# Kernel tuning notes

Hardware: AMD Instinct MI355X
Metric: run time of the kernel (lower is better)

Reference implementation:

```python
import jax, jax.numpy as jnp
import numpy as np

GAMMA = 0.1
N_CENTERS = 1024
INPUT_DIM = 64
BATCH = 65536


def setup_inputs() -> dict:
    key = jax.random.key(0)
    kx, kc = jax.random.split(key)
    x = jax.random.normal(kx, (BATCH, INPUT_DIM), dtype=jnp.float32)
    # centers ~ Uniform(0, 1), matching torch.empty(...).uniform_(0, 1)
    centers = jax.random.uniform(kc, (N_CENTERS, INPUT_DIM), dtype=jnp.float32)
    return {"x": x, "centers": centers}


def reference(x, centers):
    # Pairwise squared L2 distance via the matmul expansion trick:
    x_sq = jnp.sum(x * x, axis=-1, keepdims=True)          # [B, 1]
    c_sq = jnp.sum(centers * centers, axis=-1)             # [N]
    cross = jnp.einsum("bd,nd->bn", x, centers)            # [B, N]
    l2 = x_sq + c_sq[None, :] - 2.0 * cross                # [B, N]
    l2 = jnp.maximum(l2, 0.0)  # guard tiny negatives from the expansion
    return jnp.exp(-GAMMA * l2)
```

## Files before the change

### kernel.cpp

```cpp
#include <hip/hip_runtime.h>

#define GAMMA 0.1f

constexpr int MTOT = 65536;
constexpr int NTOT = 1024;
constexpr int KDIM = 64;
constexpr int RPB  = 256;
constexpr int SUB  = 64;
constexpr int NSUB = RPB / SUB;

using f16x8 = __attribute__((ext_vector_type(8))) _Float16;
using f16x4 = __attribute__((ext_vector_type(4))) _Float16;
using f32x4 = __attribute__((ext_vector_type(4))) float;

typedef __attribute__((address_space(1))) const unsigned int gu32;
typedef __attribute__((address_space(3))) unsigned int lu32;

constexpr size_t WS_CEN = 0;
constexpr size_t WS_CSQ = 131072;

__global__ __launch_bounds__(256)
void cen_convert_kernel(const float* __restrict__ centers,
                        _Float16* __restrict__ cen,
                        float* __restrict__ sq) {
  const int c = blockIdx.x * 256 + threadIdx.x;
  const int row = c >> 3;
  const int s = c & 7;
  const float4* p = reinterpret_cast<const float4*>(centers + (size_t)row * KDIM + s * 8);
  float4 v0 = p[0], v1 = p[1];
  const float v[8] = {v0.x, v0.y, v0.z, v0.w, v1.x, v1.y, v1.z, v1.w};
  f16x8 hv;
  float ss = 0.0f;
  #pragma unroll
  for (int i = 0; i < 8; ++i) {
    hv[i] = (_Float16)v[i];
    ss += v[i] * v[i];
  }
  ss += __shfl_xor(ss, 1);
  ss += __shfl_xor(ss, 2);
  ss += __shfl_xor(ss, 4);
  if (s == 0) sq[row] = ss;
  const int slot = s ^ (row & 7);
  *reinterpret_cast<f16x8*>(cen + (size_t)row * KDIM + slot * 8) = hv;
}

__global__ __launch_bounds__(1024, 4)
void rbf_main_kernel(const float* __restrict__ x,
                     const _Float16* __restrict__ cen,
                     const float* __restrict__ csq,
                     float* __restrict__ out) {
  __shared__ _Float16 sCen[NTOT * KDIM];
  __shared__ _Float16 sX[2][SUB * KDIM];
  __shared__ float    sCsq[NTOT];
  __shared__ float    sXsq[2][SUB];

  const int tid = threadIdx.x;
  const int mb = blockIdx.x;

  const float4* xsrc = reinterpret_cast<const float4*>(x + (size_t)mb * RPB * KDIM);

  auto convert_x = [&](float4 v4, int buf) {
    const int row = tid >> 4;
    const int f15 = tid & 15;
    const int s = f15 >> 1;
    const int half = f15 & 1;
    const float vv[4] = {v4.x, v4.y, v4.z, v4.w};
    f16x4 hv;
    float ss = 0.0f;
    #pragma unroll
    for (int e = 0; e < 4; ++e) {
      hv[e] = (_Float16)vv[e];
      ss += vv[e] * vv[e];
    }
    ss += __shfl_xor(ss, 1);
    ss += __shfl_xor(ss, 2);
    ss += __shfl_xor(ss, 4);
    ss += __shfl_xor(ss, 8);
    if (f15 == 0) sXsq[buf][row] = ss;
    const int slot = s ^ (row & 7);
    *reinterpret_cast<f16x4*>(&sX[buf][row * KDIM + slot * 8 + half * 4]) = hv;
  };

  float4 rx = xsrc[tid];
  {
    const char* src = reinterpret_cast<const char*>(cen);
    char* dst = reinterpret_cast<char*>(sCen);
    #pragma unroll
    for (int p = 0; p < 8; ++p) {
      const int q = p * 1024 + tid;
      __builtin_amdgcn_global_load_lds((gu32*)(src + (size_t)q * 16),
                                       (lu32*)(dst + (size_t)q * 16), 16, 0, 0);
    }
  }
  if (tid < 256) {
    __builtin_amdgcn_global_load_lds(
        (gu32*)(reinterpret_cast<const char*>(csq) + (size_t)tid * 16),
        (lu32*)(reinterpret_cast<char*>(sCsq) + (size_t)tid * 16), 16, 0, 0);
  }
  convert_x(rx, 0);
  rx = xsrc[1024 + tid];
  asm volatile("s_waitcnt vmcnt(1)" ::: "memory");
  asm volatile("s_waitcnt lgkmcnt(0)" ::: "memory");
  __builtin_amdgcn_s_barrier();
  __builtin_amdgcn_sched_barrier(0);

  const int lane = tid & 63;
  const int wave = tid >> 6;
  const int wm = wave & 3;
  const int wn = wave >> 2;
  const int l = lane & 15;
  const int g = lane >> 4;

  #pragma unroll 1
  for (int jt = 0; jt < NSUB; ++jt) {
    const int b = jt & 1;

    if (jt + 1 < NSUB) convert_x(rx, b ^ 1);
    if (jt + 2 < NSUB) rx = xsrc[(jt + 2) * 1024 + tid];

    const int xrow = wm * 16 + l;
    f16x8 xh[2];
    #pragma unroll
    for (int ks = 0; ks < 2; ++ks) {
      const int slot = (ks * 4 + g) ^ (l & 7);
      xh[ks] = *reinterpret_cast<const f16x8*>(&sX[b][xrow * KDIM + slot * 8]);
    }
    const float xs = sXsq[b][xrow];

    f32x4 acc[16] = {};
    #pragma unroll
    for (int ks = 0; ks < 2; ++ks) {
      const int slot = (ks * 4 + g) ^ (l & 7);
      #pragma unroll
      for (int nf = 0; nf < 16; ++nf) {
        const int crow = wn * 256 + nf * 16 + l;
        const f16x8 ch = *reinterpret_cast<const f16x8*>(&sCen[crow * KDIM + slot * 8]);
        acc[nf] = __builtin_amdgcn_mfma_f32_16x16x32_f16(ch, xh[ks], acc[nf], 0, 0, 0);
      }
    }

    const size_t rowg = (size_t)mb * RPB + jt * SUB + wm * 16 + l;
    float* orow = out + rowg * (size_t)NTOT + wn * 256;
    #pragma unroll
    for (int nf = 0; nf < 16; ++nf) {
      const float4 cs = *reinterpret_cast<const float4*>(&sCsq[wn * 256 + nf * 16 + g * 4]);
      const f32x4 a = acc[nf];
      float4 o;
      o.x = __expf(-GAMMA * fmaxf(xs + cs.x - 2.0f * a[0], 0.0f));
      o.y = __expf(-GAMMA * fmaxf(xs + cs.y - 2.0f * a[1], 0.0f));
      o.z = __expf(-GAMMA * fmaxf(xs + cs.z - 2.0f * a[2], 0.0f));
      o.w = __expf(-GAMMA * fmaxf(xs + cs.w - 2.0f * a[3], 0.0f));
      *reinterpret_cast<float4*>(orow + nf * 16 + g * 4) = o;
    }

    if (jt + 1 < NSUB) {
      asm volatile("s_waitcnt lgkmcnt(0)" ::: "memory");
      __builtin_amdgcn_s_barrier();
      __builtin_amdgcn_sched_barrier(0);
    }
  }
}

extern "C" void kernel_launch(void* const* d_in, const int* in_sizes, int n_in,
                              void* d_out, int out_size, void* d_ws, size_t ws_size,
                              hipStream_t stream) {
  (void)in_sizes; (void)n_in; (void)out_size; (void)ws_size;
  const float* x       = (const float*)d_in[0];
  const float* centers = (const float*)d_in[1];
  float* out = (float*)d_out;

  char* ws = (char*)d_ws;
  _Float16* cen = (_Float16*)(ws + WS_CEN);
  float*    csq = (float*)(ws + WS_CSQ);

  cen_convert_kernel<<<32, 256, 0, stream>>>(centers, cen, csq);
  rbf_main_kernel<<<MTOT / RPB, 1024, 0, stream>>>(x, cen, csq, out);
}
```

Before: 60.31 us.

## Fuse center conversion into main kernel and shrink sub-tile to 32 rows

Drops the separate center-conversion launch: every block now loads fp32 centers, converts them to fp16 with the swizzle and computes squared norms directly into LDS. The row sub-tile shrinks from 64 to 32, so waves are remapped to 2x8 and each wave covers 128 centers. The MFMA loop is reordered so each 16-center fragment is accumulated and written out immediately, which cuts accumulator register pressure. In exchange, each of the 256 blocks redundantly reads and converts 256KB of fp32 centers, and the double-buffered x pipeline runs more iterations with only half the threads loading.

```diff
diff --git a/kernel.cpp b/kernel.cpp
--- a/kernel.cpp
+++ b/kernel.cpp
@@ -6,49 +6,17 @@
 constexpr int NTOT = 1024;
 constexpr int KDIM = 64;
 constexpr int RPB  = 256;
-constexpr int SUB  = 64;
+constexpr int SUB  = 32;
 constexpr int NSUB = RPB / SUB;
 
 using f16x8 = __attribute__((ext_vector_type(8))) _Float16;
 using f16x4 = __attribute__((ext_vector_type(4))) _Float16;
 using f32x4 = __attribute__((ext_vector_type(4))) float;
 
-typedef __attribute__((address_space(1))) const unsigned int gu32;
-typedef __attribute__((address_space(3))) unsigned int lu32;
-
-constexpr size_t WS_CEN = 0;
-constexpr size_t WS_CSQ = 131072;
-
-__global__ __launch_bounds__(256)
-void cen_convert_kernel(const float* __restrict__ centers,
-                        _Float16* __restrict__ cen,
-                        float* __restrict__ sq) {
-  const int c = blockIdx.x * 256 + threadIdx.x;
-  const int row = c >> 3;
-  const int s = c & 7;
-  const float4* p = reinterpret_cast<const float4*>(centers + (size_t)row * KDIM + s * 8);
-  float4 v0 = p[0], v1 = p[1];
-  const float v[8] = {v0.x, v0.y, v0.z, v0.w, v1.x, v1.y, v1.z, v1.w};
-  f16x8 hv;
-  float ss = 0.0f;
-  #pragma unroll
-  for (int i = 0; i < 8; ++i) {
-    hv[i] = (_Float16)v[i];
-    ss += v[i] * v[i];
-  }
-  ss += __shfl_xor(ss, 1);
-  ss += __shfl_xor(ss, 2);
-  ss += __shfl_xor(ss, 4);
-  if (s == 0) sq[row] = ss;
-  const int slot = s ^ (row & 7);
-  *reinterpret_cast<f16x8*>(cen + (size_t)row * KDIM + slot * 8) = hv;
-}
-
 __global__ __launch_bounds__(1024, 4)
-void rbf_main_kernel(const float* __restrict__ x,
-                     const _Float16* __restrict__ cen,
-                     const float* __restrict__ csq,
-                     float* __restrict__ out) {
+void rbf_fused_kernel(const float* __restrict__ x,
+                      const float* __restrict__ centers,
+                      float* __restrict__ out) {
   __shared__ _Float16 sCen[NTOT * KDIM];
   __shared__ _Float16 sX[2][SUB * KDIM];
   __shared__ float    sCsq[NTOT];
@@ -81,33 +49,44 @@
     *reinterpret_cast<f16x4*>(&sX[buf][row * KDIM + slot * 8 + half * 4]) = hv;
   };
 
-  float4 rx = xsrc[tid];
+  float4 rx;
+  if (tid < 512) rx = xsrc[tid];
+
   {
-    const char* src = reinterpret_cast<const char*>(cen);
-    char* dst = reinterpret_cast<char*>(sCen);
+    const float4* cf = reinterpret_cast<const float4*>(centers);
     #pragma unroll
     for (int p = 0; p < 8; ++p) {
-      const int q = p * 1024 + tid;
-      __builtin_amdgcn_global_load_lds((gu32*)(src + (size_t)q * 16),
-                                       (lu32*)(dst + (size_t)q * 16), 16, 0, 0);
+      const int c = p * 1024 + tid;
+      const int row = c >> 3;
+      const int s = c & 7;
+      const float4 v0 = cf[c * 2];
+      const float4 v1 = cf[c * 2 + 1];
+      const float v[8] = {v0.x, v0.y, v0.z, v0.w, v1.x, v1.y, v1.z, v1.w};
+      f16x8 hv;
+      float ss = 0.0f;
+      #pragma unroll
+      for (int i = 0; i < 8; ++i) {
+        hv[i] = (_Float16)v[i];
+        ss += v[i] * v[i];
+      }
+      ss += __shfl_xor(ss, 1);
+      ss += __shfl_xor(ss, 2);
+      ss += __shfl_xor(ss, 4);
+      if (s == 0) sCsq[row] = ss;
+      const int slot = s ^ (row & 7);
+      *reinterpret_cast<f16x8*>(&sCen[row * KDIM + slot * 8]) = hv;
     }
   }
-  if (tid < 256) {
-    __builtin_amdgcn_global_load_lds(
-        (gu32*)(reinterpret_cast<const char*>(csq) + (size_t)tid * 16),
-        (lu32*)(reinterpret_cast<char*>(sCsq) + (size_t)tid * 16), 16, 0, 0);
+  if (tid < 512) {
+    convert_x(rx, 0);
+    rx = xsrc[512 + tid];
   }
-  convert_x(rx, 0);
-  rx = xsrc[1024 + tid];
-  asm volatile("s_waitcnt vmcnt(1)" ::: "memory");
-  asm volatile("s_waitcnt lgkmcnt(0)" ::: "memory");
-  __builtin_amdgcn_s_barrier();
-  __builtin_amdgcn_sched_barrier(0);
+  __syncthreads();
 
   const int lane = tid & 63;
   const int wave = tid >> 6;
-  const int wm = wave & 3;
-  const int wn = wave >> 2;
+  const int wm = wave & 1;
+  const int wn = wave >> 1;
   const int l = lane & 15;
   const int g = lane >> 4;
 
@@ -115,8 +94,8 @@
   for (int jt = 0; jt < NSUB; ++jt) {
     const int b = jt & 1;
 
-    if (jt + 1 < NSUB) convert_x(rx, b ^ 1);
-    if (jt + 2 < NSUB) rx = xsrc[(jt + 2) * 1024 + tid];
+    if (jt + 1 < NSUB && tid < 512) convert_x(rx, b ^ 1);
+    if (jt + 2 < NSUB && tid < 512) rx = xsrc[(jt + 2) * 512 + tid];
 
     const int xrow = wm * 16 + l;
     f16x8 xh[2];
@@ -127,29 +106,25 @@
     }
     const float xs = sXsq[b][xrow];
 
-    f32x4 acc[16] = {};
+    const size_t rowg = (size_t)mb * RPB + jt * SUB + wm * 16 + l;
+    float* orow = out + rowg * (size_t)NTOT + wn * 128;
+
     #pragma unroll
-    for (int ks = 0; ks < 2; ++ks) {
-      const int slot = (ks * 4 + g) ^ (l & 7);
+    for (int nf = 0; nf < 8; ++nf) {
+      const int crow = wn * 128 + nf * 16 + l;
+      f32x4 acc = {};
       #pragma unroll
-      for (int nf = 0; nf < 16; ++nf) {
-        const int crow = wn * 256 + nf * 16 + l;
+      for (int ks = 0; ks < 2; ++ks) {
+        const int slot = (ks * 4 + g) ^ (l & 7);
         const f16x8 ch = *reinterpret_cast<const f16x8*>(&sCen[crow * KDIM + slot * 8]);
-        acc[nf] = __builtin_amdgcn_mfma_f32_16x16x32_f16(ch, xh[ks], acc[nf], 0, 0, 0);
+        acc = __builtin_amdgcn_mfma_f32_16x16x32_f16(ch, xh[ks], acc, 0, 0, 0);
       }
-    }
-
-    const size_t rowg = (size_t)mb * RPB + jt * SUB + wm * 16 + l;
-    float* orow = out + rowg * (size_t)NTOT + wn * 256;
-    #pragma unroll
-    for (int nf = 0; nf < 16; ++nf) {
-      const float4 cs = *reinterpret_cast<const float4*>(&sCsq[wn * 256 + nf * 16 + g * 4]);
-      const f32x4 a = acc[nf];
+      const float4 cs = *reinterpret_cast<const float4*>(&sCsq[wn * 128 + nf * 16 + g * 4]);
       float4 o;
-      o.x = __expf(-GAMMA * fmaxf(xs + cs.x - 2.0f * a[0], 0.0f));
-      o.y = __expf(-GAMMA * fmaxf(xs + cs.y - 2.0f * a[1], 0.0f));
-      o.z = __expf(-GAMMA * fmaxf(xs + cs.z - 2.0f * a[2], 0.0f));
-      o.w = __expf(-GAMMA * fmaxf(xs + cs.w - 2.0f * a[3], 0.0f));
+      o.x = __expf(-GAMMA * fmaxf(xs + cs.x - 2.0f * acc[0], 0.0f));
+      o.y = __expf(-GAMMA * fmaxf(xs + cs.y - 2.0f * acc[1], 0.0f));
+      o.z = __expf(-GAMMA * fmaxf(xs + cs.z - 2.0f * acc[2], 0.0f));
+      o.w = __expf(-GAMMA * fmaxf(xs + cs.w - 2.0f * acc[3], 0.0f));
       *reinterpret_cast<float4*>(orow + nf * 16 + g * 4) = o;
     }
 
@@ -164,15 +139,9 @@
 extern "C" void kernel_launch(void* const* d_in, const int* in_sizes, int n_in,
                               void* d_out, int out_size, void* d_ws, size_t ws_size,
                               hipStream_t stream) {
-  (void)in_sizes; (void)n_in; (void)out_size; (void)ws_size;
+  (void)in_sizes; (void)n_in; (void)d_ws; (void)ws_size; (void)out_size;
   const float* x       = (const float*)d_in[0];
   const float* centers = (const float*)d_in[1];
   float* out = (float*)d_out;
-
-  char* ws = (char*)d_ws;
-  _Float16* cen = (_Float16*)(ws + WS_CEN);
-  float*    csq = (float*)(ws + WS_CSQ);
-
-  cen_convert_kernel<<<32, 256, 0, stream>>>(centers, cen, csq);
-  rbf_main_kernel<<<MTOT / RPB, 1024, 0, stream>>>(x, cen, csq, out);
+  rbf_fused_kernel<<<MTOT / RPB, 1024, 0, stream>>>(x, centers, out);
 }
```

Result: no change. 59.39 us (-1.5%).
